# Optimization experiments

Measured on AMD Instinct MI355X. Metric: run time of the kernel, lower is better.

## Reference

```python
import jax, jax.numpy as jnp
import numpy as np

D_QK = 32  # out_channels // 8


def conv1x1(x, w, b):
    # x: [B,C,H,W], w: [O,C], b: [O] -> [B,O,H,W]
    return jnp.einsum('bchw,oc->bohw', x, w) + b[None, :, None, None]


def setup_inputs() -> dict:
    key = jax.random.key(0)
    ks = jax.random.split(key, 10)
    B, C, H, W = 4, 256, 64, 64
    in_ch, out_ch, attn_ch = 512, 256, 256
    s_in = 1.0 / np.sqrt(in_ch)
    s_at = 1.0 / np.sqrt(attn_ch)
    return {
        'ef': jax.random.normal(ks[0], (B, C, H, W), jnp.float32),
        'sf': jax.random.normal(ks[1], (B, C, H, W), jnp.float32),
        'Attn': jax.random.normal(ks[2], (B, attn_ch, H, W), jnp.float32),
        'Qw': jax.random.uniform(ks[3], (D_QK, in_ch), jnp.float32, -s_in, s_in),
        'Qb': jax.random.uniform(ks[4], (D_QK,), jnp.float32, -s_in, s_in),
        'Kw': jax.random.uniform(ks[5], (D_QK, attn_ch), jnp.float32, -s_at, s_at),
        'Kb': jax.random.uniform(ks[6], (D_QK,), jnp.float32, -s_at, s_at),
        'Vw': jax.random.uniform(ks[7], (out_ch, in_ch), jnp.float32, -s_in, s_in),
        'Vb': jax.random.uniform(ks[8], (out_ch,), jnp.float32, -s_in, s_in),
        'gamma': jnp.ones((1,), jnp.float32) * 0.25,
    }


def reference(ef, sf, Attn, Qw, Qb, Kw, Kb, Vw, Vb, gamma):
    B, C, H, W = ef.shape
    N = H * W
    x = jnp.concatenate((ef, sf), axis=1)  # [B, 2C, H, W]
    q = conv1x1(x, Qw, Qb).reshape(B, D_QK, N)         # [B, d, N]
    k = conv1x1(Attn, Kw, Kb).reshape(B, D_QK, N)      # [B, d, N]
    # scores[b, m, n] = sum_d q[b, d, m] * k[b, d, n]  (no 1/sqrt(d) scale)
    scores = jnp.einsum('bdm,bdn->bmn', q, k)
    attn = jax.nn.softmax(scores, axis=-1)             # [B, N, N]
    v = conv1x1(x, Vw, Vb).reshape(B, C, N)            # [B, C, N]
    # out[b, c, m] = sum_n v[b, c, n] * attn[b, m, n]
    out = jnp.einsum('bcn,bmn->bcm', v, attn).reshape(B, C, H, W)
    return gamma[0] * out + ef
```

## Files before the change

### kernel.cpp

```cpp
#include <hip/hip_runtime.h>
#include <hip/hip_bf16.h>

typedef short bf16x8 __attribute__((ext_vector_type(8)));
typedef float f32x4 __attribute__((ext_vector_type(4)));

#define MFMA16(a, b, c) __builtin_amdgcn_mfma_f32_16x16x32_bf16(a, b, c, 0, 0, 0)

#define NB 4
#define NC 256
#define NSP 4096
#define LOG2E 1.4426950408889634f

__device__ __forceinline__ unsigned short f2bf(float f) {
    return (unsigned short)((__float_as_uint(f) + 0x8000u) >> 16);
}
__device__ __forceinline__ unsigned pk2bf(float hi, float lo) {
    return __builtin_amdgcn_perm(__float_as_uint(hi) + 0x8000u,
                                 __float_as_uint(lo) + 0x8000u, 0x07060302u);
}

__global__ __launch_bounds__(256) void prep_w(
    const float* __restrict__ Qw, const float* __restrict__ Kw,
    const float* __restrict__ Vw,
    unsigned short* __restrict__ Qwbf, unsigned short* __restrict__ Kwbf,
    unsigned short* __restrict__ Vwbf)
{
    int i = blockIdx.x * 256 + threadIdx.x;
    {
        const float4* vs = (const float4*)(Vw + (size_t)i * 8);
        float4 a = vs[0], c = vs[1];
        int4 st;
        st.x = (int)pk2bf(a.y, a.x); st.y = (int)pk2bf(a.w, a.z);
        st.z = (int)pk2bf(c.y, c.x); st.w = (int)pk2bf(c.w, c.z);
        *(int4*)(Vwbf + (size_t)i * 8) = st;
    }
    if (i < 2048) {
        const float4* qs = (const float4*)(Qw + (size_t)i * 8);
        float4 a = qs[0], c = qs[1];
        int4 st;
        st.x = (int)pk2bf(a.y, a.x); st.y = (int)pk2bf(a.w, a.z);
        st.z = (int)pk2bf(c.y, c.x); st.w = (int)pk2bf(c.w, c.z);
        *(int4*)(Qwbf + (size_t)i * 8) = st;
    }
    if (i < 1024) {
        const float4* ks = (const float4*)(Kw + (size_t)i * 8);
        float4 a = ks[0], c = ks[1];
        int4 st;
        st.x = (int)pk2bf(a.y, a.x); st.y = (int)pk2bf(a.w, a.z);
        st.z = (int)pk2bf(c.y, c.x); st.w = (int)pk2bf(c.w, c.z);
        *(int4*)(Kwbf + (size_t)i * 8) = st;
    }
}

__global__ __launch_bounds__(256) void proj_fused(
    const float* __restrict__ ef, const float* __restrict__ sf,
    const float* __restrict__ attnp,
    const unsigned short* __restrict__ Qwbf, const float* __restrict__ Qb,
    const unsigned short* __restrict__ Kwbf, const float* __restrict__ Kb,
    const unsigned short* __restrict__ Vwbf, const float* __restrict__ Vb,
    unsigned short* __restrict__ qws, unsigned short* __restrict__ kws,
    unsigned short* __restrict__ vws)
{
    __shared__ __align__(16) unsigned short xt[32][72];

    int t = threadIdx.x;
    int w = t >> 6, lane = t & 63, quad = lane >> 4, l15 = lane & 15;
    int b = blockIdx.y;
    int ci = t & 63, sm = t >> 6;
    int mi = w >> 1, oh = w & 1;

    if (blockIdx.x < 128) {
        int mt = blockIdx.x, m0 = mt * 32;

        f32x4 zero = {0.f, 0.f, 0.f, 0.f};
        f32x4 acc[2][4];
#pragma unroll
        for (int m = 0; m < 2; ++m)
#pragma unroll
            for (int ot = 0; ot < 4; ++ot) acc[m][ot] = zero;
        f32x4 qacc = zero;

        const float* s0p = ef + ((size_t)(b * NC) + ci) * NSP + m0 + sm * 8;
        float4 x0 = *(const float4*)s0p;
        float4 x1 = *(const float4*)(s0p + 4);

        for (int c = 0; c < 8; ++c) {
            float4 n0 = x0, n1 = x1;
            if (c < 7) {
                int cn = c + 1;
                const float* sn = (cn < 4 ? ef : sf) +
                                  ((size_t)(b * NC) + (cn & 3) * 64 + ci) * NSP + m0 + sm * 8;
                n0 = *(const float4*)sn;
                n1 = *(const float4*)(sn + 4);
            }
            __syncthreads();
            unsigned short* xd = &xt[sm * 8][ci];
            xd[0]   = f2bf(x0.x); xd[72]  = f2bf(x0.y);
            xd[144] = f2bf(x0.z); xd[216] = f2bf(x0.w);
            xd[288] = f2bf(x1.x); xd[360] = f2bf(x1.y);
            xd[432] = f2bf(x1.z); xd[504] = f2bf(x1.w);
            __syncthreads();
            int ci0 = c * 64;
#pragma unroll
            for (int ks = 0; ks < 2; ++ks) {
                bf16x8 a0 = *(const bf16x8*)&xt[l15][ks * 32 + quad * 8];
                bf16x8 a1 = *(const bf16x8*)&xt[16 + l15][ks * 32 + quad * 8];
                bf16x8 bq = *(const bf16x8*)(Qwbf + (size_t)(oh * 16 + l15) * 512 + ci0 + ks * 32 + quad * 8);
                qacc = MFMA16(mi ? a1 : a0, bq, qacc);
#pragma unroll
                for (int ot = 0; ot < 4; ++ot) {
                    bf16x8 bv = *(const bf16x8*)(Vwbf + (size_t)(w * 64 + ot * 16 + l15) * 512 + ci0 + ks * 32 + quad * 8);
                    acc[0][ot] = MFMA16(a0, bv, acc[0][ot]);
                    acc[1][ot] = MFMA16(a1, bv, acc[1][ot]);
                }
            }
            x0 = n0; x1 = n1;
        }

#pragma unroll
        for (int ot = 0; ot < 4; ++ot) {
            int ch = w * 64 + ot * 16 + l15;
            float bias = Vb[ch];
            unsigned* vp = (unsigned*)(vws + ((size_t)((b * 128 + mt) * 256 + ch)) * 32);
#pragma unroll
            for (int r = 0; r < 4; ++r)
                vp[quad * 4 + r] = pk2bf(acc[1][ot][r] + bias, acc[0][ot][r] + bias);
        }

        int o = oh * 16 + l15;
        float bb = Qb[o];
#pragma unroll
        for (int r = 0; r < 4; ++r) {
            int m = m0 + mi * 16 + quad * 4 + r;
            qws[((size_t)(b * NSP) + m) * 32 + o] = f2bf((qacc[r] + bb) * LOG2E);
        }
    } else {
        int mt = blockIdx.x - 128, m0 = mt * 32;

        f32x4 acc = {0.f, 0.f, 0.f, 0.f};

        const float* s0p = attnp + ((size_t)(b * NC) + ci) * NSP + m0 + sm * 8;
        float4 x0 = *(const float4*)s0p;
        float4 x1 = *(const float4*)(s0p + 4);

        for (int c = 0; c < 4; ++c) {
            float4 n0 = x0, n1 = x1;
            if (c < 3) {
                const float* sn = attnp + ((size_t)(b * NC) + (c + 1) * 64 + ci) * NSP + m0 + sm * 8;
                n0 = *(const float4*)sn;
                n1 = *(const float4*)(sn + 4);
            }
            __syncthreads();
            unsigned short* xd = &xt[sm * 8][ci];
            xd[0]   = f2bf(x0.x); xd[72]  = f2bf(x0.y);
            xd[144] = f2bf(x0.z); xd[216] = f2bf(x0.w);
            xd[288] = f2bf(x1.x); xd[360] = f2bf(x1.y);
            xd[432] = f2bf(x1.z); xd[504] = f2bf(x1.w);
            __syncthreads();
            int ci0 = c * 64;
#pragma unroll
            for (int ks = 0; ks < 2; ++ks) {
                bf16x8 a  = *(const bf16x8*)&xt[mi * 16 + l15][ks * 32 + quad * 8];
                bf16x8 bk = *(const bf16x8*)(Kwbf + (size_t)(oh * 16 + l15) * 256 + ci0 + ks * 32 + quad * 8);
                acc = MFMA16(a, bk, acc);
            }
            x0 = n0; x1 = n1;
        }

        int o = oh * 16 + l15;
        float bb = Kb[o];
#pragma unroll
        for (int r = 0; r < 4; ++r) {
            int m = m0 + mi * 16 + quad * 4 + r;
            kws[((size_t)(b * NSP) + m) * 32 + o] = f2bf(acc[r] + bb);
        }
    }
}

__global__ __launch_bounds__(512, 2) void attention(
    const unsigned short* __restrict__ qws, const unsigned short* __restrict__ kws,
    const unsigned short* __restrict__ vws, const float* __restrict__ ef,
    const float* __restrict__ gamma, float* __restrict__ out)
{
    __shared__ __align__(16) unsigned short Plds[2][2][64 * 72];
    __shared__ float denl[2][64];

    int t = threadIdx.x;
    int g = t >> 8, tl = t & 255;
    int w = tl >> 6, lane = tl & 63, quad = lane >> 4, l15 = lane & 15;
    int b = blockIdx.x >> 6, m0 = (blockIdx.x & 63) << 6;

    const unsigned short* kbase = kws + (size_t)(b * NSP) * 32;
    const unsigned short* vbase = vws + (size_t)(b * 128) * 8192;

    bf16x8 qf = *(const bf16x8*)(qws + ((size_t)(b * NSP) + m0 + w * 16 + l15) * 32 + quad * 8);

    f32x4 zero = {0.f, 0.f, 0.f, 0.f};
    f32x4 acc[4][4];
#pragma unroll
    for (int i = 0; i < 4; ++i)
#pragma unroll
        for (int j = 0; j < 4; ++j) acc[i][j] = zero;
    float lp0 = 0.f, lp1 = 0.f, lp2 = 0.f, lp3 = 0.f;

    int tt0 = g * 64;
    bf16x8 kf[4];
#pragma unroll
    for (int j = 0; j < 4; ++j)
        kf[j] = *(const bf16x8*)(kbase + (size_t)((tt0 + (j >> 1)) * 32 + (j & 1) * 16 + l15) * 32 + quad * 8);
    bf16x8 vf[2][4];
#pragma unroll
    for (int h = 0; h < 2; ++h)
#pragma unroll
        for (int cc = 0; cc < 4; ++cc)
            vf[h][cc] = *(const bf16x8*)(vbase + (size_t)(tt0 + h) * 8192 + (w * 64 + cc * 16 + l15) * 32 + quad * 8);

    for (int it = 0; it < 32; ++it) {
        int buf = it & 1;
        f32x4 s0 = MFMA16(qf, kf[0], zero);
        f32x4 s1 = MFMA16(qf, kf[1], zero);
        f32x4 s2 = MFMA16(qf, kf[2], zero);
        f32x4 s3 = MFMA16(qf, kf[3], zero);

        float e0[4], e1[4], e2[4], e3[4];
#pragma unroll
        for (int r = 0; r < 4; ++r) {
            e0[r] = __builtin_amdgcn_exp2f(s0[r]);
            e1[r] = __builtin_amdgcn_exp2f(s1[r]);
            e2[r] = __builtin_amdgcn_exp2f(s2[r]);
            e3[r] = __builtin_amdgcn_exp2f(s3[r]);
        }
        lp0 += (e0[0] + e1[0]) + (e2[0] + e3[0]);
        lp1 += (e0[1] + e1[1]) + (e2[1] + e3[1]);
        lp2 += (e0[2] + e1[2]) + (e2[2] + e3[2]);
        lp3 += (e0[3] + e1[3]) + (e2[3] + e3[3]);

        unsigned short* pd = &Plds[g][buf][(w * 16 + quad * 4) * 72 + 2 * l15];
#pragma unroll
        for (int r = 0; r < 4; ++r) {
            *(unsigned*)(pd + r * 72)      = pk2bf(e1[r], e0[r]);
            *(unsigned*)(pd + r * 72 + 32) = pk2bf(e3[r], e2[r]);
        }

        int itn = it + 1 < 32 ? it + 1 : 31;
        int ttn = tt0 + 2 * itn;
#pragma unroll
        for (int j = 0; j < 4; ++j)
            kf[j] = *(const bf16x8*)(kbase + (size_t)((ttn + (j >> 1)) * 32 + (j & 1) * 16 + l15) * 32 + quad * 8);
        bf16x8 vfn[2][4];
#pragma unroll
        for (int h = 0; h < 2; ++h)
#pragma unroll
            for (int cc = 0; cc < 4; ++cc)
                vfn[h][cc] = *(const bf16x8*)(vbase + (size_t)(ttn + h) * 8192 + (w * 64 + cc * 16 + l15) * 32 + quad * 8);

        __syncthreads();

        __builtin_amdgcn_s_setprio(1);
#pragma unroll
        for (int h = 0; h < 2; ++h) {
            bf16x8 pa0 = *(const bf16x8*)&Plds[g][buf][(0  + l15) * 72 + h * 32 + quad * 8];
            bf16x8 pa1 = *(const bf16x8*)&Plds[g][buf][(16 + l15) * 72 + h * 32 + quad * 8];
            bf16x8 pa2 = *(const bf16x8*)&Plds[g][buf][(32 + l15) * 72 + h * 32 + quad * 8];
            bf16x8 pa3 = *(const bf16x8*)&Plds[g][buf][(48 + l15) * 72 + h * 32 + quad * 8];
#pragma unroll
            for (int cc = 0; cc < 4; ++cc) {
                acc[0][cc] = MFMA16(pa0, vf[h][cc], acc[0][cc]);
                acc[1][cc] = MFMA16(pa1, vf[h][cc], acc[1][cc]);
                acc[2][cc] = MFMA16(pa2, vf[h][cc], acc[2][cc]);
                acc[3][cc] = MFMA16(pa3, vf[h][cc], acc[3][cc]);
            }
        }
        __builtin_amdgcn_s_setprio(0);
#pragma unroll
        for (int h = 0; h < 2; ++h)
#pragma unroll
            for (int cc = 0; cc < 4; ++cc) vf[h][cc] = vfn[h][cc];
    }

    lp0 += __shfl_xor(lp0, 1); lp0 += __shfl_xor(lp0, 2); lp0 += __shfl_xor(lp0, 4); lp0 += __shfl_xor(lp0, 8);
    lp1 += __shfl_xor(lp1, 1); lp1 += __shfl_xor(lp1, 2); lp1 += __shfl_xor(lp1, 4); lp1 += __shfl_xor(lp1, 8);
    lp2 += __shfl_xor(lp2, 1); lp2 += __shfl_xor(lp2, 2); lp2 += __shfl_xor(lp2, 4); lp2 += __shfl_xor(lp2, 8);
    lp3 += __shfl_xor(lp3, 1); lp3 += __shfl_xor(lp3, 2); lp3 += __shfl_xor(lp3, 4); lp3 += __shfl_xor(lp3, 8);
    if (l15 == 0) {
        int base = w * 16 + quad * 4;
        denl[g][base + 0] = lp0; denl[g][base + 1] = lp1;
        denl[g][base + 2] = lp2; denl[g][base + 3] = lp3;
    }
    __syncthreads();

    float (*mrgO)[68] = (float (*)[68])&Plds[0][0][0];
    float gam = gamma[0];

#pragma unroll
    for (int half = 0; half < 2; ++half) {
        if (g == 1) {
#pragma unroll
            for (int qc = 0; qc < 4; ++qc)
#pragma unroll
                for (int c2 = 0; c2 < 2; ++c2)
                    *(f32x4*)&mrgO[w * 32 + c2 * 16 + l15][qc * 16 + quad * 4] = acc[qc][half * 2 + c2];
        }
        __syncthreads();
        if (g == 0) {
#pragma unroll
            for (int qc = 0; qc < 4; ++qc) {
                int qb = qc * 16 + quad * 4;
                float4 d0 = *(const float4*)&denl[0][qb];
                float4 d1 = *(const float4*)&denl[1][qb];
                float r0 = gam / (d0.x + d1.x), r1 = gam / (d0.y + d1.y);
                float r2 = gam / (d0.z + d1.z), r3 = gam / (d0.w + d1.w);
#pragma unroll
                for (int c2 = 0; c2 < 2; ++c2) {
                    int cc = half * 2 + c2;
                    int ch = w * 64 + cc * 16 + l15;
                    f32x4 part = *(const f32x4*)&mrgO[w * 32 + c2 * 16 + l15][qb];
                    size_t off = ((size_t)(b * NC + ch)) * NSP + m0 + qb;
                    float4 e = *(const float4*)(ef + off);
                    float4 o;
                    o.x = (acc[qc][cc][0] + part[0]) * r0 + e.x;
                    o.y = (acc[qc][cc][1] + part[1]) * r1 + e.y;
                    o.z = (acc[qc][cc][2] + part[2]) * r2 + e.z;
                    o.w = (acc[qc][cc][3] + part[3]) * r3 + e.w;
                    *(float4*)(out + off) = o;
                }
            }
        }
        __syncthreads();
    }
}

extern "C" void kernel_launch(void* const* d_in, const int* in_sizes, int n_in,
                              void* d_out, int out_size, void* d_ws, size_t ws_size,
                              hipStream_t stream) {
    const float* ef    = (const float*)d_in[0];
    const float* sf    = (const float*)d_in[1];
    const float* attn  = (const float*)d_in[2];
    const float* Qw    = (const float*)d_in[3];
    const float* Qb    = (const float*)d_in[4];
    const float* Kw    = (const float*)d_in[5];
    const float* Kb    = (const float*)d_in[6];
    const float* Vw    = (const float*)d_in[7];
    const float* Vb    = (const float*)d_in[8];
    const float* gamma = (const float*)d_in[9];
    float* out = (float*)d_out;

    unsigned short* qws  = (unsigned short*)d_ws;
    unsigned short* kws  = qws + (size_t)4 * 4096 * 32;
    unsigned short* vws  = kws + (size_t)4 * 4096 * 32;
    unsigned short* Qwbf = vws + (size_t)4 * 128 * 256 * 32;
    unsigned short* Kwbf = Qwbf + 32 * 512;
    unsigned short* Vwbf = Kwbf + 32 * 256;

    hipLaunchKernelGGL(prep_w, dim3(64), dim3(256), 0, stream,
                       Qw, Kw, Vw, Qwbf, Kwbf, Vwbf);
    hipLaunchKernelGGL(proj_fused, dim3(256, 4), dim3(256), 0, stream,
                       ef, sf, attn, Qwbf, Qb, Kwbf, Kb, Vwbf, Vb, qws, kws, vws);
    hipLaunchKernelGGL(attention, dim3(256), dim3(512), 0, stream,
                       qws, kws, vws, ef, gamma, out);
}
```

Before: 190.5 us.

## Halve attention query tile to double grid and split key work across waves

The attention kernel now handles 32 query rows per block instead of 64, giving 512 blocks, and launch bounds ask for 4 blocks per CU instead of 2. Each wave now computes scores for one 16-row query half and one 32-key half, and the denominators are reduced across the two key halves. The aim is more parallelism, higher occupancy and fewer registers per wave. The cost is that every block re-reads the full K and V streams, doubling global traffic for V. Separately, the projection kernel now interleaves the Q/V and K block roles by blockIdx parity, and the s_setprio hints are removed.

```diff
diff --git a/kernel.cpp b/kernel.cpp
--- a/kernel.cpp
+++ b/kernel.cpp
@@ -68,10 +68,10 @@
     int b = blockIdx.y;
     int ci = t & 63, sm = t >> 6;
     int mi = w >> 1, oh = w & 1;
-
-    if (blockIdx.x < 128) {
-        int mt = blockIdx.x, m0 = mt * 32;
-
+    int role = blockIdx.x & 1;
+    int mt = blockIdx.x >> 1, m0 = mt * 32;
+
+    if (role == 0) {
         f32x4 zero = {0.f, 0.f, 0.f, 0.f};
         f32x4 acc[2][4];
 #pragma unroll
@@ -135,8 +135,6 @@
             qws[((size_t)(b * NSP) + m) * 32 + o] = f2bf((qacc[r] + bb) * LOG2E);
         }
     } else {
-        int mt = blockIdx.x - 128, m0 = mt * 32;
-
         f32x4 acc = {0.f, 0.f, 0.f, 0.f};
 
         const float* s0p = attnp + ((size_t)(b * NC) + ci) * NSP + m0 + sm * 8;
@@ -177,101 +175,89 @@
     }
 }
 
-__global__ __launch_bounds__(512, 2) void attention(
+__global__ __launch_bounds__(512, 4) void attention(
     const unsigned short* __restrict__ qws, const unsigned short* __restrict__ kws,
     const unsigned short* __restrict__ vws, const float* __restrict__ ef,
     const float* __restrict__ gamma, float* __restrict__ out)
 {
-    __shared__ __align__(16) unsigned short Plds[2][2][64 * 72];
-    __shared__ float denl[2][64];
+    __shared__ __align__(16) unsigned short Plds[2][2][32 * 72];
+    __shared__ __align__(16) float denl[2][2][32];
 
     int t = threadIdx.x;
     int g = t >> 8, tl = t & 255;
     int w = tl >> 6, lane = tl & 63, quad = lane >> 4, l15 = lane & 15;
-    int b = blockIdx.x >> 6, m0 = (blockIdx.x & 63) << 6;
+    int qh = w & 1, kh = w >> 1;
+    int b = blockIdx.x >> 7, m0 = (blockIdx.x & 127) << 5;
 
     const unsigned short* kbase = kws + (size_t)(b * NSP) * 32;
     const unsigned short* vbase = vws + (size_t)(b * 128) * 8192;
 
-    bf16x8 qf = *(const bf16x8*)(qws + ((size_t)(b * NSP) + m0 + w * 16 + l15) * 32 + quad * 8);
+    bf16x8 qf = *(const bf16x8*)(qws + ((size_t)(b * NSP) + m0 + qh * 16 + l15) * 32 + quad * 8);
 
     f32x4 zero = {0.f, 0.f, 0.f, 0.f};
-    f32x4 acc[4][4];
-#pragma unroll
-    for (int i = 0; i < 4; ++i)
+    f32x4 acc[2][4];
+#pragma unroll
+    for (int i = 0; i < 2; ++i)
 #pragma unroll
         for (int j = 0; j < 4; ++j) acc[i][j] = zero;
     float lp0 = 0.f, lp1 = 0.f, lp2 = 0.f, lp3 = 0.f;
 
-    int tt0 = g * 64;
-    bf16x8 kf[4];
-#pragma unroll
-    for (int j = 0; j < 4; ++j)
-        kf[j] = *(const bf16x8*)(kbase + (size_t)((tt0 + (j >> 1)) * 32 + (j & 1) * 16 + l15) * 32 + quad * 8);
+    bf16x8 kf[2];
+#pragma unroll
+    for (int j = 0; j < 2; ++j)
+        kf[j] = *(const bf16x8*)(kbase + (size_t)((g * 64 + kh) * 32 + j * 16 + l15) * 32 + quad * 8);
     bf16x8 vf[2][4];
 #pragma unroll
     for (int h = 0; h < 2; ++h)
 #pragma unroll
         for (int cc = 0; cc < 4; ++cc)
-            vf[h][cc] = *(const bf16x8*)(vbase + (size_t)(tt0 + h) * 8192 + (w * 64 + cc * 16 + l15) * 32 + quad * 8);
+            vf[h][cc] = *(const bf16x8*)(vbase + (size_t)(g * 64 + h) * 8192 + (w * 64 + cc * 16 + l15) * 32 + quad * 8);
 
     for (int it = 0; it < 32; ++it) {
         int buf = it & 1;
         f32x4 s0 = MFMA16(qf, kf[0], zero);
         f32x4 s1 = MFMA16(qf, kf[1], zero);
-        f32x4 s2 = MFMA16(qf, kf[2], zero);
-        f32x4 s3 = MFMA16(qf, kf[3], zero);
-
-        float e0[4], e1[4], e2[4], e3[4];
+
+        float e0[4], e1[4];
 #pragma unroll
         for (int r = 0; r < 4; ++r) {
             e0[r] = __builtin_amdgcn_exp2f(s0[r]);
             e1[r] = __builtin_amdgcn_exp2f(s1[r]);
-            e2[r] = __builtin_amdgcn_exp2f(s2[r]);
-            e3[r] = __builtin_amdgcn_exp2f(s3[r]);
-        }
-        lp0 += (e0[0] + e1[0]) + (e2[0] + e3[0]);
-        lp1 += (e0[1] + e1[1]) + (e2[1] + e3[1]);
-        lp2 += (e0[2] + e1[2]) + (e2[2] + e3[2]);
-        lp3 += (e0[3] + e1[3]) + (e2[3] + e3[3]);
-
-        unsigned short* pd = &Plds[g][buf][(w * 16 + quad * 4) * 72 + 2 * l15];
-#pragma unroll
-        for (int r = 0; r < 4; ++r) {
-            *(unsigned*)(pd + r * 72)      = pk2bf(e1[r], e0[r]);
-            *(unsigned*)(pd + r * 72 + 32) = pk2bf(e3[r], e2[r]);
-        }
+        }
+        lp0 += e0[0] + e1[0];
+        lp1 += e0[1] + e1[1];
+        lp2 += e0[2] + e1[2];
+        lp3 += e0[3] + e1[3];
+
+        unsigned short* pd = &Plds[g][buf][(qh * 16 + quad * 4) * 72 + kh * 32 + 2 * l15];
+#pragma unroll
+        for (int r = 0; r < 4; ++r)
+            *(unsigned*)(pd + r * 72) = pk2bf(e1[r], e0[r]);
 
         int itn = it + 1 < 32 ? it + 1 : 31;
-        int ttn = tt0 + 2 * itn;
-#pragma unroll
-        for (int j = 0; j < 4; ++j)
-            kf[j] = *(const bf16x8*)(kbase + (size_t)((ttn + (j >> 1)) * 32 + (j & 1) * 16 + l15) * 32 + quad * 8);
+        int Tn = g * 64 + 2 * itn;
+#pragma unroll
+        for (int j = 0; j < 2; ++j)
+            kf[j] = *(const bf16x8*)(kbase + (size_t)((Tn + kh) * 32 + j * 16 + l15) * 32 + quad * 8);
         bf16x8 vfn[2][4];
 #pragma unroll
         for (int h = 0; h < 2; ++h)
 #pragma unroll
             for (int cc = 0; cc < 4; ++cc)
-                vfn[h][cc] = *(const bf16x8*)(vbase + (size_t)(ttn + h) * 8192 + (w * 64 + cc * 16 + l15) * 32 + quad * 8);
+                vfn[h][cc] = *(const bf16x8*)(vbase + (size_t)(Tn + h) * 8192 + (w * 64 + cc * 16 + l15) * 32 + quad * 8);
 
         __syncthreads();
 
-        __builtin_amdgcn_s_setprio(1);
 #pragma unroll
         for (int h = 0; h < 2; ++h) {
             bf16x8 pa0 = *(const bf16x8*)&Plds[g][buf][(0  + l15) * 72 + h * 32 + quad * 8];
             bf16x8 pa1 = *(const bf16x8*)&Plds[g][buf][(16 + l15) * 72 + h * 32 + quad * 8];
-            bf16x8 pa2 = *(const bf16x8*)&Plds[g][buf][(32 + l15) * 72 + h * 32 + quad * 8];
-            bf16x8 pa3 = *(const bf16x8*)&Plds[g][buf][(48 + l15) * 72 + h * 32 + quad * 8];
 #pragma unroll
             for (int cc = 0; cc < 4; ++cc) {
                 acc[0][cc] = MFMA16(pa0, vf[h][cc], acc[0][cc]);
                 acc[1][cc] = MFMA16(pa1, vf[h][cc], acc[1][cc]);
-                acc[2][cc] = MFMA16(pa2, vf[h][cc], acc[2][cc]);
-                acc[3][cc] = MFMA16(pa3, vf[h][cc], acc[3][cc]);
-            }
-        }
-        __builtin_amdgcn_s_setprio(0);
+            }
+        }
 #pragma unroll
         for (int h = 0; h < 2; ++h)
 #pragma unroll
@@ -283,33 +269,37 @@
     lp2 += __shfl_xor(lp2, 1); lp2 += __shfl_xor(lp2, 2); lp2 += __shfl_xor(lp2, 4); lp2 += __shfl_xor(lp2, 8);
     lp3 += __shfl_xor(lp3, 1); lp3 += __shfl_xor(lp3, 2); lp3 += __shfl_xor(lp3, 4); lp3 += __shfl_xor(lp3, 8);
     if (l15 == 0) {
-        int base = w * 16 + quad * 4;
-        denl[g][base + 0] = lp0; denl[g][base + 1] = lp1;
-        denl[g][base + 2] = lp2; denl[g][base + 3] = lp3;
+        int base = qh * 16 + quad * 4;
+        denl[g][kh][base + 0] = lp0; denl[g][kh][base + 1] = lp1;
+        denl[g][kh][base + 2] = lp2; denl[g][kh][base + 3] = lp3;
     }
     __syncthreads();
 
-    float (*mrgO)[68] = (float (*)[68])&Plds[0][0][0];
+    float (*mrgO)[36] = (float (*)[36])&Plds[0][0][0];
     float gam = gamma[0];
 
 #pragma unroll
     for (int half = 0; half < 2; ++half) {
         if (g == 1) {
 #pragma unroll
-            for (int qc = 0; qc < 4; ++qc)
+            for (int qc2 = 0; qc2 < 2; ++qc2)
 #pragma unroll
                 for (int c2 = 0; c2 < 2; ++c2)
-                    *(f32x4*)&mrgO[w * 32 + c2 * 16 + l15][qc * 16 + quad * 4] = acc[qc][half * 2 + c2];
+                    *(f32x4*)&mrgO[w * 32 + c2 * 16 + l15][qc2 * 16 + quad * 4] = acc[qc2][half * 2 + c2];
         }
         __syncthreads();
         if (g == 0) {
 #pragma unroll
-            for (int qc = 0; qc < 4; ++qc) {
-                int qb = qc * 16 + quad * 4;
-                float4 d0 = *(const float4*)&denl[0][qb];
-                float4 d1 = *(const float4*)&denl[1][qb];
-                float r0 = gam / (d0.x + d1.x), r1 = gam / (d0.y + d1.y);
-                float r2 = gam / (d0.z + d1.z), r3 = gam / (d0.w + d1.w);
+            for (int qc2 = 0; qc2 < 2; ++qc2) {
+                int qb = qc2 * 16 + quad * 4;
+                float4 d00 = *(const float4*)&denl[0][0][qb];
+                float4 d01 = *(const float4*)&denl[0][1][qb];
+                float4 d10 = *(const float4*)&denl[1][0][qb];
+                float4 d11 = *(const float4*)&denl[1][1][qb];
+                float r0 = gam / ((d00.x + d01.x) + (d10.x + d11.x));
+                float r1 = gam / ((d00.y + d01.y) + (d10.y + d11.y));
+                float r2 = gam / ((d00.z + d01.z) + (d10.z + d11.z));
+                float r3 = gam / ((d00.w + d01.w) + (d10.w + d11.w));
 #pragma unroll
                 for (int c2 = 0; c2 < 2; ++c2) {
                     int cc = half * 2 + c2;
@@ -318,10 +308,10 @@
                     size_t off = ((size_t)(b * NC + ch)) * NSP + m0 + qb;
                     float4 e = *(const float4*)(ef + off);
                     float4 o;
-                    o.x = (acc[qc][cc][0] + part[0]) * r0 + e.x;
-                    o.y = (acc[qc][cc][1] + part[1]) * r1 + e.y;
-                    o.z = (acc[qc][cc][2] + part[2]) * r2 + e.z;
-                    o.w = (acc[qc][cc][3] + part[3]) * r3 + e.w;
+                    o.x = (acc[qc2][cc][0] + part[0]) * r0 + e.x;
+                    o.y = (acc[qc2][cc][1] + part[1]) * r1 + e.y;
+                    o.z = (acc[qc2][cc][2] + part[2]) * r2 + e.z;
+                    o.w = (acc[qc2][cc][3] + part[3]) * r3 + e.w;
                     *(float4*)(out + off) = o;
                 }
             }
@@ -356,6 +346,6 @@
                        Qw, Kw, Vw, Qwbf, Kwbf, Vwbf);
     hipLaunchKernelGGL(proj_fused, dim3(256, 4), dim3(256), 0, stream,
                        ef, sf, attn, Qwbf, Qb, Kwbf, Kb, Vwbf, Vb, qws, kws, vws);
-    hipLaunchKernelGGL(attention, dim3(256), dim3(512), 0, stream,
+    hipLaunchKernelGGL(attention, dim3(512), dim3(512), 0, stream,
                        qws, kws, vws, ef, gamma, out);
 }
```

Measured after the change: 300.9 us. 58.0% more time.
